# Kernel optimization log

Hardware: AMD Instinct MI355X
Metric: run time of the kernel (lower is better)

The kernel has to match this reference:

```python
import jax, jax.numpy as jnp
import numpy as np

N_NODES = 50000
N_EDGES = 800000
IN_CH, HID_CH, OUT_CH = 256, 128, 64


def setup_inputs() -> dict:
    key = jax.random.key(0)
    k1, k2, k3, k4 = jax.random.split(key, 4)
    x = jax.random.normal(k1, (N_NODES, IN_CH), dtype=jnp.float32)
    edge_index = jax.random.randint(k2, (2, N_EDGES), 0, N_NODES, dtype=jnp.int64)
    # Glorot-style init for the GCN weight matrices, zero bias (PyG default)
    W1 = jax.random.normal(k3, (IN_CH, HID_CH), dtype=jnp.float32) * (1.0 / np.sqrt(IN_CH))
    b1 = jnp.zeros((HID_CH,), dtype=jnp.float32)
    W2 = jax.random.normal(k4, (HID_CH, OUT_CH), dtype=jnp.float32) * (1.0 / np.sqrt(HID_CH))
    b2 = jnp.zeros((OUT_CH,), dtype=jnp.float32)
    return {"x": x, "edge_index": edge_index, "W1": W1, "b1": b1, "W2": W2, "b2": b2}


def _gcn_conv(x, W, b, src, dst, dinv_sqrt, n_nodes):
    # linear transform then degree-normalized scatter-add aggregation
    h = x @ W                                        # [N, F_out]
    norm = dinv_sqrt[src] * dinv_sqrt[dst]           # [E+N]
    msg = h[src] * norm[:, None]                     # gather + scale
    out = jax.ops.segment_sum(msg, dst, num_segments=n_nodes)
    return out + b


def reference(x, edge_index, W1, b1, W2, b2):
    n_nodes = x.shape[0]
    loops = jnp.arange(n_nodes, dtype=edge_index.dtype)
    src = jnp.concatenate([edge_index[0], loops])    # add self-loops (PyG default)
    dst = jnp.concatenate([edge_index[1], loops])
    # symmetric normalization: deg computed over targets incl. self-loops
    deg = jax.ops.segment_sum(jnp.ones_like(dst, dtype=x.dtype), dst, num_segments=n_nodes)
    dinv_sqrt = jnp.where(deg > 0, jax.lax.rsqrt(deg), 0.0)
    h = jax.nn.relu(_gcn_conv(x, W1, b1, src, dst, dinv_sqrt, n_nodes))
    return _gcn_conv(h, W2, b2, src, dst, dinv_sqrt, n_nodes)
```

## Files before the change

kernel.cpp:

```cpp
#include <hip/hip_runtime.h>


typedef __attribute__((ext_vector_type(4))) float floatx4;
typedef _Float16 __attribute__((ext_vector_type(8))) half8v;

#define BUCK_SH 6
#define BUCK    64
#define NBLK    256

#define AS1(p) ((const __attribute__((address_space(1))) void*)(p))
#define AS3(p) ((__attribute__((address_space(3))) void*)(p))

__device__ __forceinline__ int edge_id(const int* __restrict__ ei, int is64, long long pos) {
    return is64 ? ei[2 * pos] : ei[(int)pos];
}

__device__ __forceinline__ int detect_is64(const int* __restrict__ ei) {
    __shared__ int nz;
    if (threadIdx.x == 0) nz = 0;
    __syncthreads();
    if (threadIdx.x < 256 && ei[2 * threadIdx.x + 1] != 0) atomicOr(&nz, 1);
    __syncthreads();
    return (nz == 0) ? 1 : 0;
}

__device__ __forceinline__ void convW_one(const float* W, _Float16* Wt, int K, int Nc, int idx) {
    if (idx >= K * Nc) return;
    int k = idx / Nc, n = idx % Nc;
    Wt[(long long)n * K + k] = (_Float16)W[idx];
}

__global__ void __launch_bounds__(256)
hist2convW_kernel(const int* __restrict__ ei, int* __restrict__ hist2,
                  int E, int NB, int chunk,
                  const float* __restrict__ W1, _Float16* __restrict__ W1t,
                  const float* __restrict__ W2, _Float16* __restrict__ W2t) {
    __shared__ int h[1024];
    const int t = threadIdx.x;
    const int is64 = detect_is64(ei);
    for (int i = t; i < NB; i += 256) h[i] = 0;
    __syncthreads();
    const int lo = blockIdx.x * chunk;
    const int hi = min(E, lo + chunk);
    for (int e = lo + t; e < hi; e += 256) {
        int d = edge_id(ei, is64, (long long)E + e);
        atomicAdd(&h[d >> BUCK_SH], 1);
    }
    __syncthreads();
    for (int i = t; i < NB; i += 256) hist2[(long long)blockIdx.x * NB + i] = h[i];
    {
        int gtid = blockIdx.x * 256 + t;
        convW_one(W1, W1t, 256, 128, gtid);
        int g2 = gtid - 256 * 128;
        if (g2 >= 0) convW_one(W2, W2t, 128, 64, g2);
    }
}

__global__ void __launch_bounds__(256)
wavescan_kernel(const int* __restrict__ hist2, int* __restrict__ start2t,
                int* __restrict__ colsum, int NB) {
    const int wid  = (blockIdx.x * 256 + threadIdx.x) >> 6;
    const int lane = threadIdx.x & 63;
    if (wid >= NB) return;
    int carry = 0;
    for (int c = 0; c < NBLK; c += 64) {
        int v = hist2[(long long)(c + lane) * NB + wid];
        int incl = v;
#pragma unroll
        for (int s = 1; s < 64; s <<= 1) {
            int u = __shfl_up(incl, s, 64);
            if (lane >= s) incl += u;
        }
        start2t[(long long)wid * NBLK + c + lane] = carry + incl - v;
        carry += __shfl(incl, 63, 64);
    }
    if (lane == 0) colsum[wid] = carry;
}

__global__ void __launch_bounds__(1024)
basescan_kernel(const int* __restrict__ colsum, int* __restrict__ bbase, int NB, int E) {
    __shared__ int sm[1024];
    const int t = threadIdx.x;
    int v = (t < NB) ? colsum[t] : 0;
    sm[t] = v;
    __syncthreads();
    for (int s = 1; s < 1024; s <<= 1) {
        int u = (t >= s) ? sm[t - s] : 0;
        __syncthreads();
        sm[t] += u;
        __syncthreads();
    }
    if (t < NB) bbase[t] = sm[t] - v;
    if (t == 0) bbase[NB] = E;
}

__global__ void __launch_bounds__(256)
scatter2_kernel(const int* __restrict__ ei, const int* __restrict__ bbase,
                const int* __restrict__ start2t, unsigned* __restrict__ ebuf,
                int E, int NB, int chunk) {
    __shared__ int hcur[1024];
    const int t = threadIdx.x;
    const int is64 = detect_is64(ei);
    for (int i = t; i < NB; i += 256)
        hcur[i] = bbase[i] + start2t[(long long)i * NBLK + blockIdx.x];
    __syncthreads();
    const int lo = blockIdx.x * chunk;
    const int hi = min(E, lo + chunk);
    for (int e = lo + t; e < hi; e += 256) {
        int s = edge_id(ei, is64, e);
        int d = edge_id(ei, is64, (long long)E + e);
        int pos = atomicAdd(&hcur[d >> BUCK_SH], 1);
        ebuf[pos] = (unsigned)s | ((unsigned)(d & (BUCK - 1)) << 26);
    }
}

__global__ void __launch_bounds__(256)
csrbuild_kernel(const unsigned* __restrict__ ebuf, const int* __restrict__ bbase,
                int* __restrict__ offs, float* __restrict__ dinv,
                int* __restrict__ csr, int N, int NB, int E) {
    __shared__ int cnt[BUCK], exc[BUCK], cur[BUCK];
    const int b = blockIdx.x;
    const int t = threadIdx.x;
    if (t < BUCK) { cnt[t] = 0; cur[t] = 0; }
    __syncthreads();
    const int lo = bbase[b], hi = bbase[b + 1];
    for (int i = lo + t; i < hi; i += blockDim.x)
        atomicAdd(&cnt[ebuf[i] >> 26], 1);
    __syncthreads();
    if (t == 0) {
        int run = 0;
        for (int l = 0; l < BUCK; ++l) { exc[l] = run; run += cnt[l]; }
    }
    __syncthreads();
    if (t < BUCK) {
        int n = b * BUCK + t;
        if (n < N) {
            offs[n] = lo + exc[t];
            dinv[n] = rsqrtf(1.0f + (float)cnt[t]);
        }
    }
    if (b == NB - 1 && t == 0) offs[N] = E;
    for (int i = lo + t; i < hi; i += blockDim.x) {
        unsigned e = ebuf[i];
        int l = e >> 26;
        int p = lo + exc[l] + atomicAdd(&cur[l], 1);
        csr[p] = (int)(e & 0x03FFFFFFu);
    }
}

template <int NCOL, int K>
__launch_bounds__(256)
__global__ void gemm_f16_kernel(const float* __restrict__ A,
                                const _Float16* __restrict__ Bt,
                                _Float16* __restrict__ C, int M) {
    constexpr int NCB = NCOL / 16;
    constexpr int BM = 128, BK = 64;
    constexpr int NC = K / BK;
    constexpr int UNITS = BM * BK / 4;
    __shared__ float As[2][BM * BK];

    const int tid  = threadIdx.x;
    const int wave = tid >> 6;
    const int lane = tid & 63;
    const int n15  = lane & 15;
    const int q    = lane >> 4;
    const int row0 = blockIdx.x * BM;

    floatx4 acc[2][NCB];
#pragma unroll
    for (int rt = 0; rt < 2; ++rt)
#pragma unroll
        for (int c = 0; c < NCB; ++c) acc[rt][c] = (floatx4){0.f, 0.f, 0.f, 0.f};

    auto stage = [&](int buf, int kc) {
#pragma unroll
        for (int j = 0; j < UNITS / 256; ++j) {
            int g = j * 256 + tid;
            int r = g >> 4;
            int u = (g & 15) ^ (r & 15);
            int gr = row0 + r;
            if (gr >= M) gr = M - 1;
            const float* gp = &A[(long long)gr * K + kc + u * 4];
            float* lp = &As[buf][g * 4];
            __builtin_amdgcn_global_load_lds(AS1(gp), AS3(lp), 16, 0, 0);
        }
    };

    stage(0, 0);
    __syncthreads();

#pragma unroll
    for (int c = 0; c < NC; ++c) {
        if (c + 1 < NC) stage((c + 1) & 1, (c + 1) * BK);
        const int buf = c & 1;
#pragma unroll
        for (int ks = 0; ks < 2; ++ks) {
            half8v af[2];
#pragma unroll
            for (int rt = 0; rt < 2; ++rt) {
                const int R = wave * 32 + rt * 16 + n15;
                const int u0 = ks * 8 + q * 2;
                const int p0 = (u0)     ^ (R & 15);
                const int p1 = (u0 + 1) ^ (R & 15);
                float4 f0 = *(const float4*)&As[buf][R * BK + p0 * 4];
                float4 f1 = *(const float4*)&As[buf][R * BK + p1 * 4];
                af[rt][0] = (_Float16)f0.x; af[rt][1] = (_Float16)f0.y;
                af[rt][2] = (_Float16)f0.z; af[rt][3] = (_Float16)f0.w;
                af[rt][4] = (_Float16)f1.x; af[rt][5] = (_Float16)f1.y;
                af[rt][6] = (_Float16)f1.z; af[rt][7] = (_Float16)f1.w;
            }
#pragma unroll
            for (int cb = 0; cb < NCB; ++cb) {
                const _Float16* bp = &Bt[(long long)(cb * 16 + n15) * K + c * BK + ks * 32 + q * 8];
                half8v bf = *(const half8v*)bp;
                acc[0][cb] = __builtin_amdgcn_mfma_f32_16x16x32_f16(af[0], bf, acc[0][cb], 0, 0, 0);
                acc[1][cb] = __builtin_amdgcn_mfma_f32_16x16x32_f16(af[1], bf, acc[1][cb], 0, 0, 0);
            }
        }
        if (c + 1 < NC) __syncthreads();
    }

#pragma unroll
    for (int rt = 0; rt < 2; ++rt) {
#pragma unroll
        for (int cb = 0; cb < NCB; ++cb) {
            int col = cb * 16 + n15;
#pragma unroll
            for (int r = 0; r < 4; ++r) {
                int gr = row0 + wave * 32 + rt * 16 + q * 4 + r;
                if (gr < M) C[(long long)gr * NCOL + col] = (_Float16)acc[rt][cb][r];
            }
        }
    }
}

template <int F, int RELU>
__launch_bounds__(256)
__global__ void gatherh_kernel(const _Float16* __restrict__ h, const int* __restrict__ csr,
                               const int* __restrict__ offs, const float* __restrict__ dinv,
                               const float* __restrict__ bias, float* __restrict__ out, int N) {
    constexpr int L = F / 8;
    constexpr int NPB = 256 / L;
    const int n = blockIdx.x * NPB + threadIdx.x / L;
    const int c8 = (threadIdx.x % L) * 8;
    if (n >= N) return;

    const float di = dinv[n];
    half8v hs = *(const half8v*)&h[(long long)n * F + c8];
    float acc[8];
    const float sd = di * di;
#pragma unroll
    for (int j = 0; j < 8; ++j) acc[j] = (float)hs[j] * sd;

    const int end = offs[n + 1];
    for (int j = offs[n]; j < end; j += 8) {
        int s[8];
        float ws[8];
        half8v v[8];
#pragma unroll
        for (int u = 0; u < 8; ++u) {
            int jj = j + u;
            s[u] = csr[jj < end ? jj : end - 1];
        }
#pragma unroll
        for (int u = 0; u < 8; ++u)
            ws[u] = (j + u < end) ? dinv[s[u]] * di : 0.f;
#pragma unroll
        for (int u = 0; u < 8; ++u) v[u] = *(const half8v*)&h[(long long)s[u] * F + c8];
#pragma unroll
        for (int u = 0; u < 8; ++u) {
#pragma unroll
            for (int t = 0; t < 8; ++t) acc[t] = fmaf((float)v[u][t], ws[u], acc[t]);
        }
    }

    float4 b0 = *(const float4*)&bias[c8];
    float4 b1 = *(const float4*)&bias[c8 + 4];
    float bb[8] = {b0.x, b0.y, b0.z, b0.w, b1.x, b1.y, b1.z, b1.w};
#pragma unroll
    for (int t = 0; t < 8; ++t) {
        acc[t] += bb[t];
        if (RELU) acc[t] = fmaxf(acc[t], 0.f);
    }
    float* o = &out[(long long)n * F + c8];
    *(float4*)o       = make_float4(acc[0], acc[1], acc[2], acc[3]);
    *(float4*)(o + 4) = make_float4(acc[4], acc[5], acc[6], acc[7]);
}

extern "C" void kernel_launch(void* const* d_in, const int* in_sizes, int n_in,
                              void* d_out, int out_size, void* d_ws, size_t ws_size,
                              hipStream_t stream) {
    const float* x  = (const float*)d_in[0];
    const int*   ei = (const int*)d_in[1];
    const float* W1 = (const float*)d_in[2];
    const float* b1 = (const float*)d_in[3];
    const float* W2 = (const float*)d_in[4];
    const float* b2 = (const float*)d_in[5];
    float* out = (float*)d_out;

    const int IN_CH = 256, HID = 128, OUT = 64;
    const int N = in_sizes[0] / IN_CH;
    const int E = in_sizes[1] / 2;
    const int NB = (N + BUCK - 1) / BUCK;
    const int chunk = (E + NBLK - 1) / NBLK;

    char* w = (char*)d_ws;
    size_t off_b = 0;
    auto alloc = [&](size_t bytes) { void* p = w + off_b; off_b = (off_b + bytes + 255) & ~(size_t)255; return p; };
    int*   hist2   = (int*)alloc((size_t)NBLK * NB * 4);
    int*   start2t = (int*)alloc((size_t)NB * NBLK * 4);
    int*   colsum  = (int*)alloc((size_t)NB * 4);
    int*   bbase   = (int*)alloc((size_t)(NB + 1) * 4);
    int*   offs    = (int*)alloc((size_t)(N + 1) * 4);
    float* dinv    = (float*)alloc((size_t)N * 4);
    unsigned* ebuf = (unsigned*)alloc((size_t)E * 4);
    int*   csr     = (int*)alloc((size_t)E * 4);
    _Float16* W1t  = (_Float16*)alloc((size_t)IN_CH * HID * 2);
    _Float16* W2t  = (_Float16*)alloc((size_t)HID * OUT * 2);
    _Float16* h1   = (_Float16*)alloc((size_t)N * HID * 2);
    float* agg1    = (float*)alloc((size_t)N * HID * 4);
    _Float16* h2   = h1;

    hist2convW_kernel<<<NBLK, 256, 0, stream>>>(ei, hist2, E, NB, chunk,
                                                W1, W1t, W2, W2t);
    wavescan_kernel<<<(NB * 64 + 255) / 256, 256, 0, stream>>>(hist2, start2t, colsum, NB);
    basescan_kernel<<<1, 1024, 0, stream>>>(colsum, bbase, NB, E);
    scatter2_kernel<<<NBLK, 256, 0, stream>>>(ei, bbase, start2t, ebuf, E, NB, chunk);
    csrbuild_kernel<<<NB, 256, 0, stream>>>(ebuf, bbase, offs, dinv, csr, N, NB, E);

    gemm_f16_kernel<128, 256><<<(N + 127) / 128, 256, 0, stream>>>(x, W1t, h1, N);
    gatherh_kernel<128, 1><<<(N * 16 + 255) / 256, 256, 0, stream>>>(h1, csr, offs, dinv, b1, agg1, N);
    gemm_f16_kernel<64, 128><<<(N + 127) / 128, 256, 0, stream>>>(agg1, W2t, h2, N);
    gatherh_kernel<64, 0><<<(N * 8 + 255) / 256, 256, 0, stream>>>(h2, csr, offs, dinv, b2, out, N);
}
```

Before: 215.1 us.

## Fuse layer-1 aggregation with layer-2 GEMM via shared-memory MFMA tile

Replaces the separate layer-1 gather kernel and layer-2 GEMM with one kernel. Each 256-thread block aggregates 16 nodes' 128-wide features with bias and ReLU, writes them as f16 to a swizzled shared tile, and one wave multiplies the tile by W2 with MFMA to produce h2 directly. This removes the fp32 agg1 round trip through global memory and one kernel launch. In exchange, only a quarter of the block does the MFMA work, it waits on a block barrier, and the per-edge gather is now unrolled by 8 with clamped indices.

```diff
diff --git a/kernel.cpp b/kernel.cpp
--- a/kernel.cpp
+++ b/kernel.cpp
@@ -229,6 +229,101 @@
             for (int r = 0; r < 4; ++r) {
                 int gr = row0 + wave * 32 + rt * 16 + q * 4 + r;
                 if (gr < M) C[(long long)gr * NCOL + col] = (_Float16)acc[rt][cb][r];
+            }
+        }
+    }
+}
+
+__launch_bounds__(256)
+__global__ void gatherg2_kernel(const _Float16* __restrict__ h,
+                                const int* __restrict__ csr,
+                                const int* __restrict__ offs,
+                                const float* __restrict__ dinv,
+                                const float* __restrict__ bias,
+                                const _Float16* __restrict__ Bt,
+                                _Float16* __restrict__ C,
+                                int N) {
+    constexpr int F = 128;
+    constexpr int NCOL = 64;
+    constexpr int L = F / 8;
+    constexpr int NPB = 256 / L;
+    __shared__ _Float16 Ash[NPB * F];
+
+    const int r  = threadIdx.x / L;
+    const int l  = threadIdx.x % L;
+    const int c8 = l * 8;
+    const int n  = blockIdx.x * NPB + r;
+
+    float acc[8];
+    if (n < N) {
+        const float di = dinv[n];
+        half8v hs = *(const half8v*)&h[(long long)n * F + c8];
+        const float sd = di * di;
+#pragma unroll
+        for (int j = 0; j < 8; ++j) acc[j] = (float)hs[j] * sd;
+
+        const int end = offs[n + 1];
+        for (int j = offs[n]; j < end; j += 8) {
+            int s[8];
+            float ws[8];
+            half8v v[8];
+#pragma unroll
+            for (int u = 0; u < 8; ++u) {
+                int jj = j + u;
+                s[u] = csr[jj < end ? jj : end - 1];
+            }
+#pragma unroll
+            for (int u = 0; u < 8; ++u)
+                ws[u] = (j + u < end) ? dinv[s[u]] * di : 0.f;
+#pragma unroll
+            for (int u = 0; u < 8; ++u) v[u] = *(const half8v*)&h[(long long)s[u] * F + c8];
+#pragma unroll
+            for (int u = 0; u < 8; ++u) {
+#pragma unroll
+                for (int t = 0; t < 8; ++t) acc[t] = fmaf((float)v[u][t], ws[u], acc[t]);
+            }
+        }
+        float4 b0 = *(const float4*)&bias[c8];
+        float4 b1v = *(const float4*)&bias[c8 + 4];
+        float bb[8] = {b0.x, b0.y, b0.z, b0.w, b1v.x, b1v.y, b1v.z, b1v.w};
+#pragma unroll
+        for (int t = 0; t < 8; ++t) acc[t] = fmaxf(acc[t] + bb[t], 0.f);
+    } else {
+#pragma unroll
+        for (int t = 0; t < 8; ++t) acc[t] = 0.f;
+    }
+
+    half8v hv;
+#pragma unroll
+    for (int t = 0; t < 8; ++t) hv[t] = (_Float16)acc[t];
+    *(half8v*)&Ash[(r * 16 + (l ^ r)) * 8] = hv;
+    __syncthreads();
+
+    if (threadIdx.x < 64) {
+        const int lane = threadIdx.x;
+        const int n15 = lane & 15;
+        const int q   = lane >> 4;
+        floatx4 acc2[4];
+#pragma unroll
+        for (int cb = 0; cb < 4; ++cb) acc2[cb] = (floatx4){0.f, 0.f, 0.f, 0.f};
+#pragma unroll
+        for (int kc = 0; kc < 4; ++kc) {
+            const int u = (kc * 4 + q) ^ n15;
+            half8v af = *(const half8v*)&Ash[(n15 * 16 + u) * 8];
+#pragma unroll
+            for (int cb = 0; cb < 4; ++cb) {
+                const _Float16* bp = &Bt[(long long)(cb * 16 + n15) * F + kc * 32 + q * 8];
+                half8v bf = *(const half8v*)bp;
+                acc2[cb] = __builtin_amdgcn_mfma_f32_16x16x32_f16(af, bf, acc2[cb], 0, 0, 0);
+            }
+        }
+#pragma unroll
+        for (int cb = 0; cb < 4; ++cb) {
+            int col = cb * 16 + n15;
+#pragma unroll
+            for (int rr = 0; rr < 4; ++rr) {
+                int gr = blockIdx.x * NPB + q * 4 + rr;
+                if (gr < N) C[(long long)gr * NCOL + col] = (_Float16)acc2[cb][rr];
             }
         }
     }
@@ -318,8 +413,7 @@
     _Float16* W1t  = (_Float16*)alloc((size_t)IN_CH * HID * 2);
     _Float16* W2t  = (_Float16*)alloc((size_t)HID * OUT * 2);
     _Float16* h1   = (_Float16*)alloc((size_t)N * HID * 2);
-    float* agg1    = (float*)alloc((size_t)N * HID * 4);
-    _Float16* h2   = h1;
+    _Float16* h2   = (_Float16*)alloc((size_t)N * OUT * 2);
 
     hist2convW_kernel<<<NBLK, 256, 0, stream>>>(ei, hist2, E, NB, chunk,
                                                 W1, W1t, W2, W2t);
@@ -329,7 +423,6 @@
     csrbuild_kernel<<<NB, 256, 0, stream>>>(ebuf, bbase, offs, dinv, csr, N, NB, E);
 
     gemm_f16_kernel<128, 256><<<(N + 127) / 128, 256, 0, stream>>>(x, W1t, h1, N);
-    gatherh_kernel<128, 1><<<(N * 16 + 255) / 256, 256, 0, stream>>>(h1, csr, offs, dinv, b1, agg1, N);
-    gemm_f16_kernel<64, 128><<<(N + 127) / 128, 256, 0, stream>>>(agg1, W2t, h2, N);
+    gatherg2_kernel<<<(N + 15) / 16, 256, 0, stream>>>(h1, csr, offs, dinv, b1, W2t, h2, N);
     gatherh_kernel<64, 0><<<(N * 8 + 255) / 256, 256, 0, stream>>>(h2, csr, offs, dinv, b2, out, N);
 }
```

New measurement: 210.3 us. -2.2%, faster.
